# Optimization experiments

Hardware: AMD Instinct MI355X
Metric: run time of the kernel (lower is better)

Reference implementation:

```python
import math
import jax, jax.numpy as jnp
import numpy as np

D_EMBD = 1024
N_HEAD = 16
BLOCK = 2048
B, T = 4, 2048


def setup_inputs() -> dict:
    key = jax.random.key(0)
    ks = jax.random.split(key, 5)
    d = D_EMBD
    return {
        "x": jax.random.normal(ks[0], (B, T, d), dtype=jnp.float32),
        "Wq": jax.random.normal(ks[1], (d, d), dtype=jnp.float32),
        "bq": jnp.zeros((d,), dtype=jnp.float32),
        "Wk": jax.random.normal(ks[2], (d, d), dtype=jnp.float32),
        "bk": jnp.zeros((d,), dtype=jnp.float32),
        "Wv": jax.random.normal(ks[3], (d, d), dtype=jnp.float32),
        "bv": jnp.zeros((d,), dtype=jnp.float32),
        "Wp": jax.random.normal(ks[4], (d, d), dtype=jnp.float32),
        "bp": jnp.zeros((d,), dtype=jnp.float32),
    }


def reference(x, Wq, bq, Wk, bk, Wv, bv, Wp, bp):
    Bb, Tt, C = x.shape
    n_head = N_HEAD
    hd = C // n_head  # head dim
    # QKV projections -> [B, H, T, hd]
    def split_heads(y):
        return y.reshape(Bb, Tt, n_head, hd).transpose(0, 2, 1, 3)
    Q = split_heads(x @ Wq + bq)
    K = split_heads(x @ Wk + bk)
    V = split_heads(x @ Wv + bv)
    # scores [B, H, T, T]
    attn = jnp.einsum('bhqd,bhkd->bhqk', Q, K) / math.sqrt(hd)
    # causal mask: -inf strictly above diagonal (matches triu(ones*-inf, 1))
    causal = jnp.tril(jnp.ones((Tt, Tt), dtype=bool))
    attn = jnp.where(causal, attn, -jnp.inf)
    attn = jax.nn.softmax(attn, axis=-1)
    y = jnp.einsum('bhqk,bhkd->bhqd', attn, V)
    y = y.transpose(0, 2, 1, 3).reshape(Bb, Tt, C)
    return y @ Wp + bp
```

## Files before the change

kernel.cpp:

```cpp
#include <hip/hip_runtime.h>
#include <stdint.h>
#include <stddef.h>

#define TT 2048
#define CC 1024
#define BBATCH 4
#define HH 16
#define HD 64
#define MTOT (BBATCH * TT)

typedef __bf16 bf16_t;
typedef __bf16 bf16x4 __attribute__((ext_vector_type(4)));
typedef __bf16 bf16x8 __attribute__((ext_vector_type(8)));
typedef float f32x4 __attribute__((ext_vector_type(4)));
typedef float f32x16 __attribute__((ext_vector_type(16)));

typedef const __attribute__((address_space(1))) uint32_t* as1_u32p;
typedef __attribute__((address_space(3))) uint32_t* as3_u32p;

__device__ __forceinline__ f32x4 mfma16(bf16x8 a, bf16x8 b, f32x4 c) {
  return __builtin_amdgcn_mfma_f32_16x16x32_bf16(a, b, c, 0, 0, 0);
}
__device__ __forceinline__ f32x16 mfma32(bf16x8 a, bf16x8 b, f32x16 c) {
  return __builtin_amdgcn_mfma_f32_32x32x16_bf16(a, b, c, 0, 0, 0);
}

__device__ __forceinline__ void gload_lds16(void* lds, const void* g) {
  __builtin_amdgcn_global_load_lds((as1_u32p)g, (as3_u32p)lds, 16, 0, 0);
}

__device__ __forceinline__ bf16x8 rd32(const char* t, int row, int lane) {
  int sl = (lane >> 4) ^ ((row >> 1) & 3);
  return *(const bf16x8*)(t + row * 64 + sl * 16);
}
__device__ __forceinline__ bf16x8 rd32r(const char* t, int row, int slot) {
  return *(const bf16x8*)(t + row * 128 + ((slot ^ (row & 7)) * 16));
}

__global__ void split_x_kernel(const float* __restrict__ x, bf16_t* __restrict__ xh,
                               bf16_t* __restrict__ xl, int n4) {
  int stride = gridDim.x * blockDim.x;
  for (int i = blockIdx.x * blockDim.x + threadIdx.x; i < n4; i += stride) {
    float4 v = ((const float4*)x)[i];
    float vv[4] = {v.x, v.y, v.z, v.w};
    bf16x4 hv, lv;
#pragma unroll
    for (int j = 0; j < 4; ++j) {
      bf16_t h = (bf16_t)vv[j];
      hv[j] = h;
      lv[j] = (bf16_t)(vv[j] - (float)h);
    }
    *(bf16x4*)(xh + (size_t)i * 4) = hv;
    *(bf16x4*)(xl + (size_t)i * 4) = lv;
  }
}

__global__ void transpose_split_kernel(const float* __restrict__ Wq, const float* __restrict__ Wk,
                                       const float* __restrict__ Wv, const float* __restrict__ Wp,
                                       bf16_t* __restrict__ wqkh, bf16_t* __restrict__ wqkl,
                                       bf16_t* __restrict__ wv_t, bf16_t* __restrict__ wp_t) {
  __shared__ float tile[32][33];
  int mat = blockIdx.z;
  const float* W = (mat == 0) ? Wq : (mat == 1) ? Wk : (mat == 2) ? Wv : Wp;
  int tx = threadIdx.x, ty = threadIdx.y;
  int n0 = blockIdx.x * 32, k0 = blockIdx.y * 32;
#pragma unroll
  for (int j = 0; j < 32; j += 8)
    tile[ty + j][tx] = W[(size_t)(k0 + ty + j) * CC + n0 + tx];
  __syncthreads();
#pragma unroll
  for (int j = 0; j < 32; j += 8) {
    float v = tile[tx][ty + j];
    int n = n0 + ty + j, k = k0 + tx;
    if (mat <= 1) {
      bf16_t h = (bf16_t)v;
      size_t o = (size_t)(mat * CC + n) * CC + k;
      wqkh[o] = h;
      wqkl[o] = (bf16_t)(v - (float)h);
    } else {
      bf16_t* dst = (mat == 2) ? wv_t : wp_t;
      dst[(size_t)n * CC + k] = (bf16_t)v;
    }
  }
}

__global__ __launch_bounds__(512, 2) void gemm_qk_kernel(
    const bf16_t* __restrict__ Ah, const bf16_t* __restrict__ Al,
    const bf16_t* __restrict__ Bh, const bf16_t* __restrict__ Bl,
    const float* __restrict__ bq, const float* __restrict__ bk,
    bf16_t* __restrict__ qh, bf16_t* __restrict__ ql,
    bf16_t* __restrict__ kh, bf16_t* __restrict__ kl) {
  __shared__ __align__(16) char s_ah[2][16384];
  __shared__ __align__(16) char s_al[2][16384];
  __shared__ __align__(16) char s_bh[2][16384];
  __shared__ __align__(16) char s_bl[2][16384];

  const int blk = blockIdx.x;
  const int bn = blk & 7;
  const int bm = blk >> 3;
  const int tid = threadIdx.x, w = tid >> 6, lane = tid & 63;
  const int wr = w >> 2, wc = w & 3;
  const int qi = lane & 15, hi = lane >> 4;

  const int c0 = w * 2, c1 = w * 2 + 1;
  const int srow0 = c0 * 16 + (lane >> 2);
  const int srow1 = c1 * 16 + (lane >> 2);
  const int ssl0 = (lane & 3) ^ ((srow0 >> 1) & 3);
  const int ssl1 = (lane & 3) ^ ((srow1 >> 1) & 3);
  const size_t a_off0 = (size_t)(bm * 256 + srow0) * CC + ssl0 * 8;
  const size_t a_off1 = (size_t)(bm * 256 + srow1) * CC + ssl1 * 8;
  const size_t b_off0 = (size_t)(bn * 256 + srow0) * CC + ssl0 * 8;
  const size_t b_off1 = (size_t)(bn * 256 + srow1) * CC + ssl1 * 8;

  f32x4 acc[8][4] = {};

#define STAGE_QK(buf, k0)                                        \
  do {                                                           \
    gload_lds16(s_ah[buf] + c0 * 1024, Ah + a_off0 + (k0));      \
    gload_lds16(s_ah[buf] + c1 * 1024, Ah + a_off1 + (k0));      \
    gload_lds16(s_al[buf] + c0 * 1024, Al + a_off0 + (k0));      \
    gload_lds16(s_al[buf] + c1 * 1024, Al + a_off1 + (k0));      \
    gload_lds16(s_bh[buf] + c0 * 1024, Bh + b_off0 + (k0));      \
    gload_lds16(s_bh[buf] + c1 * 1024, Bh + b_off1 + (k0));      \
    gload_lds16(s_bl[buf] + c0 * 1024, Bl + b_off0 + (k0));      \
    gload_lds16(s_bl[buf] + c1 * 1024, Bl + b_off1 + (k0));      \
  } while (0)

  STAGE_QK(0, 0);
  int cur = 0;
  for (int ks = 0; ks < 32; ++ks) {
    if (ks < 31) {
      STAGE_QK(cur ^ 1, (ks + 1) * 32);
      asm volatile("s_waitcnt vmcnt(8)" ::: "memory");
    } else {
      asm volatile("s_waitcnt vmcnt(0)" ::: "memory");
    }
    __builtin_amdgcn_s_barrier();

    bf16x8 bfh[4], bfl[4];
#pragma unroll
    for (int ni = 0; ni < 4; ++ni) {
      int br = wc * 64 + ni * 16 + qi;
      bfh[ni] = rd32(s_bh[cur], br, lane);
      bfl[ni] = rd32(s_bl[cur], br, lane);
    }
    __builtin_amdgcn_s_setprio(1);
#pragma unroll
    for (int mi = 0; mi < 8; ++mi) {
      int ar = wr * 128 + mi * 16 + qi;
      bf16x8 ahf = rd32(s_ah[cur], ar, lane);
      bf16x8 alf = rd32(s_al[cur], ar, lane);
#pragma unroll
      for (int ni = 0; ni < 4; ++ni) {
        acc[mi][ni] = mfma16(ahf, bfh[ni], acc[mi][ni]);
        acc[mi][ni] = mfma16(ahf, bfl[ni], acc[mi][ni]);
        acc[mi][ni] = mfma16(alf, bfh[ni], acc[mi][ni]);
      }
    }
    __builtin_amdgcn_s_setprio(0);
    asm volatile("s_waitcnt lgkmcnt(0)" ::: "memory");
    __builtin_amdgcn_s_barrier();
    cur ^= 1;
  }
#undef STAGE_QK

  const int which = bn >> 2;
  const float* bias = which ? bk : bq;
  bf16_t* oh = which ? kh : qh;
  bf16_t* ol = which ? kl : ql;
#pragma unroll
  for (int mi = 0; mi < 8; ++mi) {
#pragma unroll
    for (int ni = 0; ni < 4; ++ni) {
      const int col = bn * 256 + wc * 64 + ni * 16 + qi;
      const int c1i = col & 1023;
      const int h = c1i >> 6, d = c1i & 63;
#pragma unroll
      for (int r = 0; r < 4; ++r) {
        const int row = bm * 256 + wr * 128 + mi * 16 + hi * 4 + r;
        const int b = row >> 11, t = row & 2047;
        float v = acc[mi][ni][r] + bias[c1i];
        if (!which) v *= 0.125f;
        const size_t off = ((size_t)(b * HH + h) * TT + t) * HD + d;
        bf16_t hv = (bf16_t)v;
        oh[off] = hv;
        ol[off] = (bf16_t)(v - (float)hv);
      }
    }
  }
}

template <int MODE>
__global__ __launch_bounds__(256) void gemm_kernel(
    const bf16_t* __restrict__ Ah,
    const bf16_t* __restrict__ Bh,
    const float* __restrict__ bias0,
    void* __restrict__ out0) {
  __shared__ __align__(16) char smem[2 * 8192];
  char* sAh = smem;
  char* sBh = smem + 8192;

  const int bn = blockIdx.x, bm = blockIdx.y;
  const int tid = threadIdx.x, w = tid >> 6, lane = tid & 63;
  const int wr = w >> 1, wc = w & 1;

  f32x4 acc[4][4] = {};

  for (int ks = 0; ks < 32; ++ks) {
    const int k0 = ks * 32;
    __syncthreads();
#pragma unroll
    for (int it = 0; it < 2; ++it) {
      int c = it * 4 + w;
      int row = c * 16 + (lane >> 2);
      int sl = (lane & 3) ^ ((row >> 1) & 3);
      size_t aoff = (size_t)(bm * 128 + row) * CC + k0 + sl * 8;
      size_t boff = (size_t)(bn * 128 + row) * CC + k0 + sl * 8;
      gload_lds16(sAh + c * 1024, Ah + aoff);
      gload_lds16(sBh + c * 1024, Bh + boff);
    }
    __syncthreads();

    bf16x8 afh[4], bfh[4];
#pragma unroll
    for (int i = 0; i < 4; ++i) {
      int ar = wr * 64 + i * 16 + (lane & 15);
      int br = wc * 64 + i * 16 + (lane & 15);
      afh[i] = rd32(sAh, ar, lane);
      bfh[i] = rd32(sBh, br, lane);
    }
#pragma unroll
    for (int mi = 0; mi < 4; ++mi) {
#pragma unroll
      for (int ni = 0; ni < 4; ++ni) {
        acc[mi][ni] = mfma16(afh[mi], bfh[ni], acc[mi][ni]);
      }
    }
  }

#pragma unroll
  for (int mi = 0; mi < 4; ++mi) {
#pragma unroll
    for (int ni = 0; ni < 4; ++ni) {
      const int col = bn * 128 + wc * 64 + ni * 16 + (lane & 15);
#pragma unroll
      for (int r = 0; r < 4; ++r) {
        const int row = bm * 128 + wr * 64 + mi * 16 + (lane >> 4) * 4 + r;
        float v = acc[mi][ni][r];
        if (MODE == 1) {
          const int h = col >> 6, d = col & 63;
          const int b = row >> 11, t = row & 2047;
          float vv = v + bias0[col];
          ((bf16_t*)out0)[((size_t)(b * HH + h) * HD + d) * TT + t] = (bf16_t)vv;
        } else {
          ((float*)out0)[(size_t)row * CC + col] = v + bias0[col];
        }
      }
    }
  }
}

__global__ __launch_bounds__(256, 2) void attn_kernel(
    const bf16_t* __restrict__ qh, const bf16_t* __restrict__ ql,
    const bf16_t* __restrict__ kh, const bf16_t* __restrict__ kl,
    const bf16_t* __restrict__ vt, bf16_t* __restrict__ y) {
  __shared__ __align__(16) char s_kh[2][8192];
  __shared__ __align__(16) char s_kl[2][8192];
  __shared__ __align__(16) char s_vt[2][8192];

  const int blk = blockIdx.x;
  const int bh = (blk & 7) * 8 + ((blk >> 3) & 7);
  const int p = blk >> 6;
  const int b = bh >> 4, h = bh & 15;
  const int tid = threadIdx.x, w = tid >> 6, lane = tid & 63;
  const int l31 = lane & 31, hi = lane >> 5;

  const int strow0 = w * 16 + (lane >> 3);
  const int strow1 = strow0 + 8;
  const int sl0 = (lane & 7) ^ (strow0 & 7);
  const int sl1 = (lane & 7) ^ (strow1 & 7);
  const int ksrow0 = (strow0 & ~12) | ((strow0 & 4) << 1) | ((strow0 & 8) >> 1);
  const int ksrow1 = (strow1 & ~12) | ((strow1 & 4) << 1) | ((strow1 & 8) >> 1);
  const size_t koff0 = ((size_t)bh * TT + ksrow0) * HD + sl0 * 8;
  const size_t koff1 = ((size_t)bh * TT + ksrow1) * HD + sl1 * 8;
  const size_t voff0 = ((size_t)bh * HD + strow0) * TT + sl0 * 8;
  const size_t voff1 = ((size_t)bh * HD + strow1) * TT + sl1 * 8;
  const int ch0 = (w * 2) * 1024, ch1 = (w * 2 + 1) * 1024;

#define STAGE_ATTN(buf, kt)                                                  \
  do {                                                                       \
    gload_lds16(s_kh[buf] + ch0, kh + koff0 + (size_t)(kt) * 64 * HD);       \
    gload_lds16(s_kh[buf] + ch1, kh + koff1 + (size_t)(kt) * 64 * HD);       \
    gload_lds16(s_kl[buf] + ch0, kl + koff0 + (size_t)(kt) * 64 * HD);       \
    gload_lds16(s_kl[buf] + ch1, kl + koff1 + (size_t)(kt) * 64 * HD);       \
    gload_lds16(s_vt[buf] + ch0, vt + voff0 + (size_t)(kt) * 64);            \
    gload_lds16(s_vt[buf] + ch1, vt + voff1 + (size_t)(kt) * 64);            \
  } while (0)

#pragma unroll
  for (int half = 0; half < 2; ++half) {
    const int qb = half ? (15 - p) : p;
    const int ktmax = 2 * qb + 1;
    const int qrow0 = qb * 128 + w * 32;
    const int qv = qrow0 + l31;

    bf16x8 qhf[4], qlf[4];
#pragma unroll
    for (int kc = 0; kc < 4; ++kc) {
      size_t off = ((size_t)bh * TT + qv) * HD + kc * 16 + hi * 8;
      qhf[kc] = *(const bf16x8*)(qh + off);
      qlf[kc] = *(const bf16x8*)(ql + off);
    }

    f32x16 o0 = {}, o1 = {};
    float m = -1e30f, l = 0.f;

    STAGE_ATTN(0, 0);
    int cur = 0;
    for (int kt = 0; kt <= ktmax; ++kt) {
      if (kt < ktmax) {
        STAGE_ATTN(cur ^ 1, kt + 1);
        asm volatile("s_waitcnt vmcnt(6)" ::: "memory");
      } else {
        asm volatile("s_waitcnt vmcnt(0)" ::: "memory");
      }
      __builtin_amdgcn_s_barrier();

      const char* ckh = s_kh[cur];
      const char* ckl = s_kl[cur];
      const char* cvt = s_vt[cur];
      const bool active = (qrow0 + 31 >= kt * 64);
      if (active) {
        f32x16 s0 = {}, s1 = {};
#pragma unroll
        for (int kc = 0; kc < 4; ++kc) {
          bf16x8 kfh = rd32r(ckh, l31, kc * 2 + hi);
          bf16x8 kfl = rd32r(ckl, l31, kc * 2 + hi);
          s0 = mfma32(kfh, qhf[kc], s0);
          s0 = mfma32(kfl, qhf[kc], s0);
          s0 = mfma32(kfh, qlf[kc], s0);
        }
#pragma unroll
        for (int kc = 0; kc < 4; ++kc) {
          bf16x8 kfh = rd32r(ckh, 32 + l31, kc * 2 + hi);
          bf16x8 kfl = rd32r(ckl, 32 + l31, kc * 2 + hi);
          s1 = mfma32(kfh, qhf[kc], s1);
          s1 = mfma32(kfl, qhf[kc], s1);
          s1 = mfma32(kfh, qlf[kc], s1);
        }

        if (kt * 64 + 63 > qrow0) {
#pragma unroll
          for (int r = 0; r < 16; ++r) {
            const int kvb = kt * 64 + (r & 7) + 8 * hi + 16 * (r >> 3);
            if (kvb > qv) s0[r] = -1e30f;
            if (kvb + 32 > qv) s1[r] = -1e30f;
          }
        }

        float tmax = s0[0];
#pragma unroll
        for (int r = 0; r < 16; ++r) {
          tmax = fmaxf(tmax, s0[r]);
          tmax = fmaxf(tmax, s1[r]);
        }
        tmax = fmaxf(tmax, __shfl_xor(tmax, 32));
        const float mnew = fmaxf(m, tmax);
        const float sc = __expf(m - mnew);
        float ps = 0.f;
#pragma unroll
        for (int r = 0; r < 16; ++r) {
          s0[r] = __expf(s0[r] - mnew);
          ps += s0[r];
          s1[r] = __expf(s1[r] - mnew);
          ps += s1[r];
        }
        ps += __shfl_xor(ps, 32);
        l = l * sc + ps;
        m = mnew;
#pragma unroll
        for (int r = 0; r < 16; ++r) { o0[r] *= sc; o1[r] *= sc; }

        bf16x8 pa[4];
#pragma unroll
        for (int cc = 0; cc < 4; ++cc) {
#pragma unroll
          for (int j = 0; j < 8; ++j)
            pa[cc][j] = (bf16_t)((cc >> 1) ? s1[8 * (cc & 1) + j] : s0[8 * (cc & 1) + j]);
        }

#pragma unroll
        for (int cc = 0; cc < 4; ++cc) {
          bf16x8 vf0 = rd32r(cvt, l31, cc * 2 + hi);
          bf16x8 vf1 = rd32r(cvt, 32 + l31, cc * 2 + hi);
          o0 = mfma32(vf0, pa[cc], o0);
          o1 = mfma32(vf1, pa[cc], o1);
        }
      }

      asm volatile("s_waitcnt lgkmcnt(0)" ::: "memory");
      __builtin_amdgcn_s_barrier();
      cur ^= 1;
    }

    const float inv = 1.f / l;
    bf16_t* yb = y + (size_t)(b * TT + qv) * CC + h * HD;
#pragma unroll
    for (int g = 0; g < 4; ++g) {
      bf16x4 ov0, ov1;
#pragma unroll
      for (int r = 0; r < 4; ++r) {
        ov0[r] = (bf16_t)(o0[g * 4 + r] * inv);
        ov1[r] = (bf16_t)(o1[g * 4 + r] * inv);
      }
      *(bf16x4*)(yb + g * 8 + hi * 4) = ov0;
      *(bf16x4*)(yb + 32 + g * 8 + hi * 4) = ov1;
    }
  }
#undef STAGE_ATTN
}

extern "C" void kernel_launch(void* const* d_in, const int* in_sizes, int n_in,
                              void* d_out, int out_size, void* d_ws, size_t ws_size,
                              hipStream_t stream) {
  (void)in_sizes; (void)n_in; (void)out_size; (void)ws_size;
  const float* x  = (const float*)d_in[0];
  const float* Wq = (const float*)d_in[1];
  const float* bq = (const float*)d_in[2];
  const float* Wk = (const float*)d_in[3];
  const float* bk = (const float*)d_in[4];
  const float* Wv = (const float*)d_in[5];
  const float* bv = (const float*)d_in[6];
  const float* Wp = (const float*)d_in[7];
  const float* bp = (const float*)d_in[8];

  char* ws = (char*)d_ws;
  const size_t MB = 1024 * 1024;
  bf16_t* xh   = (bf16_t*)(ws + 0 * MB);
  bf16_t* xl   = (bf16_t*)(ws + 16 * MB);
  bf16_t* wqkh = (bf16_t*)(ws + 32 * MB);
  bf16_t* wqkl = (bf16_t*)(ws + 36 * MB);
  bf16_t* wv_t = (bf16_t*)(ws + 40 * MB);
  bf16_t* wp_t = (bf16_t*)(ws + 42 * MB);
  bf16_t* qhw  = (bf16_t*)(ws + 44 * MB);
  bf16_t* qlw  = (bf16_t*)(ws + 60 * MB);
  bf16_t* khw  = (bf16_t*)(ws + 76 * MB);
  bf16_t* klw  = (bf16_t*)(ws + 92 * MB);
  bf16_t* vtw  = (bf16_t*)(ws + 108 * MB);
  bf16_t* yw   = (bf16_t*)(ws + 124 * MB);

  split_x_kernel<<<2048, 256, 0, stream>>>(x, xh, xl, MTOT * CC / 4);
  transpose_split_kernel<<<dim3(32, 32, 4), dim3(32, 8), 0, stream>>>(
      Wq, Wk, Wv, Wp, wqkh, wqkl, wv_t, wp_t);
  gemm_qk_kernel<<<256, 512, 0, stream>>>(
      xh, xl, wqkh, wqkl, bq, bk, qhw, qlw, khw, klw);
  gemm_kernel<1><<<dim3(8, 64), 256, 0, stream>>>(
      xh, wv_t, bv, vtw);
  attn_kernel<<<512, 256, 0, stream>>>(qhw, qlw, khw, klw, vtw, yw);
  gemm_kernel<2><<<dim3(8, 64), 256, 0, stream>>>(
      yw, wp_t, bp, d_out);
}
```

Before: 248.5 us.

## Split attention blocks to one query tile each, lazy rescale, tree reductions

The attention kernel no longer pairs a short and a long causal query tile per block. It launches 1024 blocks, one 128-row query tile each, ordered longest-first, and raises the occupancy hint to 3 blocks per CU. The online softmax now skips the accumulator rescale when no lane's max grew, and the max and sum reductions use a tree shape to shorten dependency chains. This trades the built-in load balance of pairing for more parallelism and dynamic scheduling. It may also add register pressure under the tighter launch bound.

```diff
diff --git a/kernel.cpp b/kernel.cpp
--- a/kernel.cpp
+++ b/kernel.cpp
@@ -260,7 +260,7 @@
   }
 }
 
-__global__ __launch_bounds__(256, 2) void attn_kernel(
+__global__ __launch_bounds__(256, 3) void attn_kernel(
     const bf16_t* __restrict__ qh, const bf16_t* __restrict__ ql,
     const bf16_t* __restrict__ kh, const bf16_t* __restrict__ kl,
     const bf16_t* __restrict__ vt, bf16_t* __restrict__ y) {
@@ -269,8 +269,8 @@
   __shared__ __align__(16) char s_vt[2][8192];
 
   const int blk = blockIdx.x;
+  const int qb = 15 - (blk >> 6);
   const int bh = (blk & 7) * 8 + ((blk >> 3) & 7);
-  const int p = blk >> 6;
   const int b = bh >> 4, h = bh & 15;
   const int tid = threadIdx.x, w = tid >> 6, lane = tid & 63;
   const int l31 = lane & 31, hi = lane >> 5;
@@ -297,125 +297,129 @@
     gload_lds16(s_vt[buf] + ch1, vt + voff1 + (size_t)(kt) * 64);            \
   } while (0)
 
-#pragma unroll
-  for (int half = 0; half < 2; ++half) {
-    const int qb = half ? (15 - p) : p;
-    const int ktmax = 2 * qb + 1;
-    const int qrow0 = qb * 128 + w * 32;
-    const int qv = qrow0 + l31;
-
-    bf16x8 qhf[4], qlf[4];
-#pragma unroll
-    for (int kc = 0; kc < 4; ++kc) {
-      size_t off = ((size_t)bh * TT + qv) * HD + kc * 16 + hi * 8;
-      qhf[kc] = *(const bf16x8*)(qh + off);
-      qlf[kc] = *(const bf16x8*)(ql + off);
-    }
-
-    f32x16 o0 = {}, o1 = {};
-    float m = -1e30f, l = 0.f;
-
-    STAGE_ATTN(0, 0);
-    int cur = 0;
-    for (int kt = 0; kt <= ktmax; ++kt) {
-      if (kt < ktmax) {
-        STAGE_ATTN(cur ^ 1, kt + 1);
-        asm volatile("s_waitcnt vmcnt(6)" ::: "memory");
-      } else {
-        asm volatile("s_waitcnt vmcnt(0)" ::: "memory");
-      }
-      __builtin_amdgcn_s_barrier();
-
-      const char* ckh = s_kh[cur];
-      const char* ckl = s_kl[cur];
-      const char* cvt = s_vt[cur];
-      const bool active = (qrow0 + 31 >= kt * 64);
-      if (active) {
-        f32x16 s0 = {}, s1 = {};
-#pragma unroll
-        for (int kc = 0; kc < 4; ++kc) {
-          bf16x8 kfh = rd32r(ckh, l31, kc * 2 + hi);
-          bf16x8 kfl = rd32r(ckl, l31, kc * 2 + hi);
-          s0 = mfma32(kfh, qhf[kc], s0);
-          s0 = mfma32(kfl, qhf[kc], s0);
-          s0 = mfma32(kfh, qlf[kc], s0);
+  const int ktmax = 2 * qb + 1;
+  const int qrow0 = qb * 128 + w * 32;
+  const int qv = qrow0 + l31;
+
+  bf16x8 qhf[4], qlf[4];
+#pragma unroll
+  for (int kc = 0; kc < 4; ++kc) {
+    size_t off = ((size_t)bh * TT + qv) * HD + kc * 16 + hi * 8;
+    qhf[kc] = *(const bf16x8*)(qh + off);
+    qlf[kc] = *(const bf16x8*)(ql + off);
+  }
+
+  f32x16 o0 = {}, o1 = {};
+  float m = -1e30f, l = 0.f;
+
+  STAGE_ATTN(0, 0);
+  int cur = 0;
+  for (int kt = 0; kt <= ktmax; ++kt) {
+    if (kt < ktmax) {
+      STAGE_ATTN(cur ^ 1, kt + 1);
+      asm volatile("s_waitcnt vmcnt(6)" ::: "memory");
+    } else {
+      asm volatile("s_waitcnt vmcnt(0)" ::: "memory");
+    }
+    __builtin_amdgcn_s_barrier();
+
+    const char* ckh = s_kh[cur];
+    const char* ckl = s_kl[cur];
+    const char* cvt = s_vt[cur];
+    const bool active = (qrow0 + 31 >= kt * 64);
+    if (active) {
+      f32x16 s0 = {}, s1 = {};
+#pragma unroll
+      for (int kc = 0; kc < 4; ++kc) {
+        bf16x8 kfh = rd32r(ckh, l31, kc * 2 + hi);
+        bf16x8 kfl = rd32r(ckl, l31, kc * 2 + hi);
+        s0 = mfma32(kfh, qhf[kc], s0);
+        s0 = mfma32(kfl, qhf[kc], s0);
+        s0 = mfma32(kfh, qlf[kc], s0);
+      }
+#pragma unroll
+      for (int kc = 0; kc < 4; ++kc) {
+        bf16x8 kfh = rd32r(ckh, 32 + l31, kc * 2 + hi);
+        bf16x8 kfl = rd32r(ckl, 32 + l31, kc * 2 + hi);
+        s1 = mfma32(kfh, qhf[kc], s1);
+        s1 = mfma32(kfl, qhf[kc], s1);
+        s1 = mfma32(kfh, qlf[kc], s1);
+      }
+
+      if (kt * 64 + 63 > qrow0) {
+#pragma unroll
+        for (int r = 0; r < 16; ++r) {
+          const int kvb = kt * 64 + (r & 7) + 8 * hi + 16 * (r >> 3);
+          if (kvb > qv) s0[r] = -1e30f;
+          if (kvb + 32 > qv) s1[r] = -1e30f;
         }
-#pragma unroll
-        for (int kc = 0; kc < 4; ++kc) {
-          bf16x8 kfh = rd32r(ckh, 32 + l31, kc * 2 + hi);
-          bf16x8 kfl = rd32r(ckl, 32 + l31, kc * 2 + hi);
-          s1 = mfma32(kfh, qhf[kc], s1);
-          s1 = mfma32(kfl, qhf[kc], s1);
-          s1 = mfma32(kfh, qlf[kc], s1);
-        }
-
-        if (kt * 64 + 63 > qrow0) {
-#pragma unroll
-          for (int r = 0; r < 16; ++r) {
-            const int kvb = kt * 64 + (r & 7) + 8 * hi + 16 * (r >> 3);
-            if (kvb > qv) s0[r] = -1e30f;
-            if (kvb + 32 > qv) s1[r] = -1e30f;
-          }
-        }
-
-        float tmax = s0[0];
-#pragma unroll
-        for (int r = 0; r < 16; ++r) {
-          tmax = fmaxf(tmax, s0[r]);
-          tmax = fmaxf(tmax, s1[r]);
-        }
-        tmax = fmaxf(tmax, __shfl_xor(tmax, 32));
-        const float mnew = fmaxf(m, tmax);
+      }
+
+      float t8[8];
+#pragma unroll
+      for (int r = 0; r < 8; ++r)
+        t8[r] = fmaxf(fmaxf(s0[r], s0[r + 8]), fmaxf(s1[r], s1[r + 8]));
+      float t4a = fmaxf(t8[0], t8[4]), t4b = fmaxf(t8[1], t8[5]);
+      float t4c = fmaxf(t8[2], t8[6]), t4d = fmaxf(t8[3], t8[7]);
+      float tmax = fmaxf(fmaxf(t4a, t4b), fmaxf(t4c, t4d));
+      tmax = fmaxf(tmax, __shfl_xor(tmax, 32));
+
+      const float mnew = fmaxf(m, tmax);
+      if (!__all(tmax <= m)) {
         const float sc = __expf(m - mnew);
-        float ps = 0.f;
-#pragma unroll
-        for (int r = 0; r < 16; ++r) {
-          s0[r] = __expf(s0[r] - mnew);
-          ps += s0[r];
-          s1[r] = __expf(s1[r] - mnew);
-          ps += s1[r];
-        }
-        ps += __shfl_xor(ps, 32);
-        l = l * sc + ps;
+        l *= sc;
+#pragma unroll
+        for (int r = 0; r < 16; ++r) { o0[r] *= sc; o1[r] *= sc; }
         m = mnew;
-#pragma unroll
-        for (int r = 0; r < 16; ++r) { o0[r] *= sc; o1[r] *= sc; }
-
-        bf16x8 pa[4];
-#pragma unroll
-        for (int cc = 0; cc < 4; ++cc) {
-#pragma unroll
-          for (int j = 0; j < 8; ++j)
-            pa[cc][j] = (bf16_t)((cc >> 1) ? s1[8 * (cc & 1) + j] : s0[8 * (cc & 1) + j]);
-        }
-
-#pragma unroll
-        for (int cc = 0; cc < 4; ++cc) {
-          bf16x8 vf0 = rd32r(cvt, l31, cc * 2 + hi);
-          bf16x8 vf1 = rd32r(cvt, 32 + l31, cc * 2 + hi);
-          o0 = mfma32(vf0, pa[cc], o0);
-          o1 = mfma32(vf1, pa[cc], o1);
-        }
-      }
-
-      asm volatile("s_waitcnt lgkmcnt(0)" ::: "memory");
-      __builtin_amdgcn_s_barrier();
-      cur ^= 1;
-    }
-
-    const float inv = 1.f / l;
-    bf16_t* yb = y + (size_t)(b * TT + qv) * CC + h * HD;
-#pragma unroll
-    for (int g = 0; g < 4; ++g) {
-      bf16x4 ov0, ov1;
-#pragma unroll
-      for (int r = 0; r < 4; ++r) {
-        ov0[r] = (bf16_t)(o0[g * 4 + r] * inv);
-        ov1[r] = (bf16_t)(o1[g * 4 + r] * inv);
-      }
-      *(bf16x4*)(yb + g * 8 + hi * 4) = ov0;
-      *(bf16x4*)(yb + 32 + g * 8 + hi * 4) = ov1;
-    }
+      }
+
+#pragma unroll
+      for (int r = 0; r < 16; ++r) {
+        s0[r] = __expf(s0[r] - m);
+        s1[r] = __expf(s1[r] - m);
+      }
+      float p8[8];
+#pragma unroll
+      for (int r = 0; r < 8; ++r)
+        p8[r] = (s0[r] + s0[r + 8]) + (s1[r] + s1[r + 8]);
+      float ps = ((p8[0] + p8[1]) + (p8[2] + p8[3])) + ((p8[4] + p8[5]) + (p8[6] + p8[7]));
+      ps += __shfl_xor(ps, 32);
+      l += ps;
+
+      bf16x8 pa[4];
+#pragma unroll
+      for (int cc = 0; cc < 4; ++cc) {
+#pragma unroll
+        for (int j = 0; j < 8; ++j)
+          pa[cc][j] = (bf16_t)((cc >> 1) ? s1[8 * (cc & 1) + j] : s0[8 * (cc & 1) + j]);
+      }
+
+#pragma unroll
+      for (int cc = 0; cc < 4; ++cc) {
+        bf16x8 vf0 = rd32r(cvt, l31, cc * 2 + hi);
+        bf16x8 vf1 = rd32r(cvt, 32 + l31, cc * 2 + hi);
+        o0 = mfma32(vf0, pa[cc], o0);
+        o1 = mfma32(vf1, pa[cc], o1);
+      }
+    }
+
+    asm volatile("s_waitcnt lgkmcnt(0)" ::: "memory");
+    __builtin_amdgcn_s_barrier();
+    cur ^= 1;
+  }
+
+  const float inv = 1.f / l;
+  bf16_t* yb = y + (size_t)(b * TT + qv) * CC + h * HD;
+#pragma unroll
+  for (int g = 0; g < 4; ++g) {
+    bf16x4 ov0, ov1;
+#pragma unroll
+    for (int r = 0; r < 4; ++r) {
+      ov0[r] = (bf16_t)(o0[g * 4 + r] * inv);
+      ov1[r] = (bf16_t)(o1[g * 4 + r] * inv);
+    }
+    *(bf16x4*)(yb + g * 8 + hi * 4) = ov0;
+    *(bf16x4*)(yb + 32 + g * 8 + hi * 4) = ov1;
   }
 #undef STAGE_ATTN
 }
@@ -456,7 +460,7 @@
       xh, xl, wqkh, wqkl, bq, bk, qhw, qlw, khw, klw);
   gemm_kernel<1><<<dim3(8, 64), 256, 0, stream>>>(
       xh, wv_t, bv, vtw);
-  attn_kernel<<<512, 256, 0, stream>>>(qhw, qlw, khw, klw, vtw, yw);
+  attn_kernel<<<1024, 256, 0, stream>>>(qhw, qlw, khw, klw, vtw, yw);
   gemm_kernel<2><<<dim3(8, 64), 256, 0, stream>>>(
       yw, wp_t, bp, d_out);
 }
```

Result: no change. 247.0 us (-0.6%).
